# Kernel tuning notes

Hardware: AMD Instinct MI355X
Metric: run time of the kernel (lower is better)

Reference implementation:

```python
import jax, jax.numpy as jnp
import numpy as np

N_TOKENS = 16384
D_MODEL = 1024
N_SEG = 4
H_SEG = 1024  # intermediate_size (4096) // num_segments


def setup_inputs() -> dict:
    key = jax.random.key(0)
    kx, ki, kg, ku, kd = jax.random.split(key, 5)
    x = jax.random.normal(kx, (N_TOKENS, D_MODEL), dtype=jnp.float32)
    token_segment_indices = jax.random.randint(ki, (N_TOKENS,), 0, N_SEG, dtype=jnp.int64)
    s = 1.0 / np.sqrt(D_MODEL)
    # weights stored [seg, in, out] for x @ W
    gate_w = jax.random.normal(kg, (N_SEG, D_MODEL, H_SEG), dtype=jnp.float32) * s
    up_w = jax.random.normal(ku, (N_SEG, D_MODEL, H_SEG), dtype=jnp.float32) * s
    down_w = jax.random.normal(kd, (N_SEG, H_SEG, D_MODEL), dtype=jnp.float32) * (1.0 / np.sqrt(H_SEG))
    return {
        'x': x,
        'gate_w': gate_w,
        'up_w': up_w,
        'down_w': down_w,
        'token_segment_indices': token_segment_indices,
    }


def reference(x, gate_w, up_w, down_w, token_segment_indices):
    # _forward_with_indices: each token is processed only by its assigned
    # segment's SwiGLU FFN; all other contributions are zero.  We compute each
    # segment densely and mask (jit-friendly, same math as gather->ffn->scatter).
    out = jnp.zeros_like(x)
    for s in range(N_SEG):
        hidden = jax.nn.silu(x @ gate_w[s]) * (x @ up_w[s])  # [N, H_SEG]
        y = hidden @ down_w[s]                                # [N, D_MODEL]
        mask = (token_segment_indices == s)[:, None]
        out = out + jnp.where(mask, y, 0.0)
    return out
```

## Files before the change

kernel.cpp:

```cpp
#include <hip/hip_runtime.h>
#include <hip/hip_bf16.h>
#include <math.h>

#define NT   16384
#define DM   1024
#define NSEG 4
#define BK   64
#define HS   1024
#define TBLN 68

typedef __attribute__((ext_vector_type(8))) short bf16x8;
typedef __attribute__((ext_vector_type(4))) float f32x4;

typedef __attribute__((address_space(1))) unsigned int gu32;
typedef __attribute__((address_space(3))) unsigned int lu32;

__device__ __forceinline__ void gll16(const void* g, void* l) {
  __builtin_amdgcn_global_load_lds((gu32*)(unsigned long long)g,
                                   (lu32*)(unsigned int)(unsigned long long)l,
                                   16, 0, 0);
}

__device__ __forceinline__ unsigned short cvt_bf16(float f) {
  unsigned int u = __float_as_uint(f);
  u += 0x7fffu + ((u >> 16) & 1u);
  return (unsigned short)(u >> 16);
}

__global__ __launch_bounds__(256) void k_prepw(
    const int* __restrict__ idx, int* __restrict__ part,
    const float* __restrict__ gw, const float* __restrict__ uw, const float* __restrict__ dw,
    unsigned short* __restrict__ gwt, unsigned short* __restrict__ uwt,
    unsigned short* __restrict__ dwt) {
  __shared__ float tile[64][65];
  const int bid = blockIdx.x, tid = threadIdx.x;
  if (bid < 64) {
    __shared__ int sc[5];
    if (tid < 5) sc[tid] = 0;
    __syncthreads();
    int lane = tid & 63;
    int w32 = idx[bid * 256 + tid];
    unsigned long long m = __ballot((tid & 1) && (w32 != 0));
    if (lane == 0 && m) atomicAdd(&sc[4], 1);
    __syncthreads();
    int is32 = (sc[4] != 0);
    int s = w32;
    if (!is32) s = idx[bid * 512 + 2 * tid];
#pragma unroll
    for (int q = 0; q < 4; ++q) {
      m = __ballot(s == q);
      if (lane == 0 && m) atomicAdd(&sc[q], (int)__popcll(m));
    }
    __syncthreads();
    if (tid < 4) part[bid * 8 + tid] = sc[tid];
    if (tid == 4) part[bid * 8 + 4] = is32;
    return;
  }
  int tb = bid - 64;
  int mtx = tb >> 10, seg = (tb >> 8) & 3, tl = tb & 255;
  const float* src = (mtx == 0 ? gw : mtx == 1 ? uw : dw) + (size_t)seg * DM * HS;
  unsigned short* dst = (mtx == 0 ? gwt : mtx == 1 ? uwt : dwt) + (size_t)seg * DM * HS;
  int n0 = (tl & 15) * 64, k0 = (tl >> 4) * 64;
  int col = tid & 63, rb = tid >> 6;
#pragma unroll
  for (int i = 0; i < 64; i += 4)
    tile[i + rb][col] = src[(size_t)(k0 + i + rb) * 1024 + n0 + col];
  __syncthreads();
  int kp = tid & 31, nb = tid >> 5;
#pragma unroll
  for (int j = 0; j < 64; j += 8) {
    int nn = j + nb;
    unsigned int w = (unsigned)cvt_bf16(tile[2 * kp][nn]) |
                     ((unsigned)cvt_bf16(tile[2 * kp + 1][nn]) << 16);
    *(unsigned int*)(dst + (size_t)(n0 + nn) * 1024 + k0 + 2 * kp) = w;
  }
}

__global__ __launch_bounds__(256) void k_cvtrank(
    const int* __restrict__ idx, const int* __restrict__ part,
    const float4* __restrict__ x,
    int* __restrict__ meta, int2* __restrict__ table,
    int* __restrict__ perm, uint4* __restrict__ xc) {
  __shared__ int cnt[64][4];
  __shared__ int wsum[4][4];
  __shared__ int tot[4], pref[4], gbase[4];
  __shared__ int rnk8[8];
  __shared__ int flag_s;
  const int tid = threadIdx.x, bid = blockIdx.x;
  const int lane = tid & 63, wv = tid >> 6;
  const int c = bid >> 5;
  const int p0 = (bid & 31) * 8;

  if (tid == 0) flag_s = part[c * 8 + 4];
  if (wv == 0) {
#pragma unroll
    for (int s = 0; s < 4; ++s) cnt[lane][s] = part[lane * 8 + s];
  }
  __syncthreads();
  const int is32 = flag_s;
  int tok = c * 256 + tid;
  int s_t = is32 ? idx[tok] : idx[2 * tok];
  int myr = 0;
  unsigned long long lt = (1ull << lane) - 1;
#pragma unroll
  for (int q = 0; q < 4; ++q) {
    unsigned long long m = __ballot(s_t == q);
    if (lane == 0) wsum[wv][q] = (int)__popcll(m);
    if (s_t == q) myr = (int)__popcll(m & lt);
  }
  __syncthreads();
  if (tid < 4) {
    int s = tid, t = 0, p = 0;
    for (int b = 0; b < 64; ++b) { if (b == c) p = t; t += cnt[b][s]; }
    tot[s] = t; pref[s] = p;
  }
  __syncthreads();
  if (tid == 0) {
    gbase[0] = 0;
    for (int s = 1; s < 4; ++s) gbase[s] = gbase[s - 1] + tot[s - 1];
    if (bid == 0) {
      int nt = 0;
      for (int s = 0; s < 4; ++s) {
        meta[s] = tot[s]; meta[5 + s] = gbase[s];
        for (int m0 = 0; m0 < tot[s]; m0 += 256) table[nt++] = make_int2(s, m0);
      }
      for (; nt < TBLN; ++nt) table[nt] = make_int2(-1, 0);
    }
  }
  __syncthreads();
  int wpre = 0;
  for (int w2 = 0; w2 < wv; ++w2) wpre += wsum[w2][s_t];
  int r = gbase[s_t] + pref[s_t] + wpre + myr;
  if (tid >= p0 && tid < p0 + 8) {
    perm[r] = tok;
    rnk8[tid - p0] = r;
  }
  __syncthreads();
  const int j = tid >> 5, l2 = tid & 31;
  const int tok8 = bid * 8 + j;
  const float4* src = x + (size_t)tok8 * 256;
  uint4* dst = xc + (size_t)rnk8[j] * 128;
#pragma unroll
  for (int it = 0; it < 4; ++it) {
    float4 a = src[it * 64 + l2 * 2];
    float4 b = src[it * 64 + l2 * 2 + 1];
    uint4 o;
    o.x = cvt_bf16(a.x) | ((unsigned)cvt_bf16(a.y) << 16);
    o.y = cvt_bf16(a.z) | ((unsigned)cvt_bf16(a.w) << 16);
    o.z = cvt_bf16(b.x) | ((unsigned)cvt_bf16(b.y) << 16);
    o.w = cvt_bf16(b.z) | ((unsigned)cvt_bf16(b.w) << 16);
    dst[it * 32 + l2] = o;
  }
}

#define WAITBAR(N) \
  asm volatile("s_waitcnt vmcnt(" #N ") lgkmcnt(0)\n\ts_barrier" ::: "memory")

#define LDF(BUF, CUR, RB, F)                                               \
  F[0][0] = *(const bf16x8*)(&BUF[CUR][((RB) + fm) * 64] + x0);            \
  F[0][1] = *(const bf16x8*)(&BUF[CUR][((RB) + fm) * 64] + x1);            \
  F[1][0] = *(const bf16x8*)(&BUF[CUR][((RB) + 16 + fm) * 64] + x0);       \
  F[1][1] = *(const bf16x8*)(&BUF[CUR][((RB) + 16 + fm) * 64] + x1);

#define MM8(ACC, MH, NH, AF, BF)                                                                                            \
  __builtin_amdgcn_s_setprio(1);                                                                                            \
  ACC[2*(MH)+0][2*(NH)+0] = __builtin_amdgcn_mfma_f32_16x16x32_bf16(AF[0][0], BF[0][0], ACC[2*(MH)+0][2*(NH)+0], 0, 0, 0);  \
  ACC[2*(MH)+0][2*(NH)+1] = __builtin_amdgcn_mfma_f32_16x16x32_bf16(AF[0][0], BF[1][0], ACC[2*(MH)+0][2*(NH)+1], 0, 0, 0);  \
  ACC[2*(MH)+1][2*(NH)+0] = __builtin_amdgcn_mfma_f32_16x16x32_bf16(AF[1][0], BF[0][0], ACC[2*(MH)+1][2*(NH)+0], 0, 0, 0);  \
  ACC[2*(MH)+1][2*(NH)+1] = __builtin_amdgcn_mfma_f32_16x16x32_bf16(AF[1][0], BF[1][0], ACC[2*(MH)+1][2*(NH)+1], 0, 0, 0);  \
  ACC[2*(MH)+0][2*(NH)+0] = __builtin_amdgcn_mfma_f32_16x16x32_bf16(AF[0][1], BF[0][1], ACC[2*(MH)+0][2*(NH)+0], 0, 0, 0);  \
  ACC[2*(MH)+0][2*(NH)+1] = __builtin_amdgcn_mfma_f32_16x16x32_bf16(AF[0][1], BF[1][1], ACC[2*(MH)+0][2*(NH)+1], 0, 0, 0);  \
  ACC[2*(MH)+1][2*(NH)+0] = __builtin_amdgcn_mfma_f32_16x16x32_bf16(AF[1][1], BF[0][1], ACC[2*(MH)+1][2*(NH)+0], 0, 0, 0);  \
  ACC[2*(MH)+1][2*(NH)+1] = __builtin_amdgcn_mfma_f32_16x16x32_bf16(AF[1][1], BF[1][1], ACC[2*(MH)+1][2*(NH)+1], 0, 0, 0);  \
  __builtin_amdgcn_s_setprio(0);

__global__ __launch_bounds__(512) void k_gateup(
    const unsigned short* __restrict__ xc,
    const unsigned short* __restrict__ gwt,
    const unsigned short* __restrict__ uwt,
    const int* __restrict__ meta,
    const int2* __restrict__ table,
    unsigned short* __restrict__ hidden) {
  __shared__ __align__(16) unsigned short As[2][256 * BK];
  __shared__ __align__(16) unsigned short Bg[2][64 * BK];
  __shared__ __align__(16) unsigned short Bu[2][64 * BK];
  const int bid = blockIdx.x, tid = threadIdx.x;
  const int2 te = table[bid >> 4];
  if (te.x < 0) return;
  const int seg = te.x, m0 = te.y;
  const int count = meta[seg], base = meta[5 + seg];
  const int n0 = (bid & 15) * 64;

  const int lane = tid & 63;
  const int wv = tid >> 6;
  const int l0 = lane >> 3, j = lane & 7;

  const int rl0 = wv * 8, rl1 = 64 + wv * 8;
  const int rb0 = (rl0 & 31) + (rl0 >> 5) * 64;
  const int rb1 = (rl1 & 31) + (rl1 >> 5) * 64;
  const int a0d0 = rb0 * 128, a0d1 = rb1 * 128;
  const int a1d0 = a0d0 + 32 * 128, a1d1 = a0d1 + 32 * 128;
  const int r00 = rb0 + l0, r01 = rb1 + l0;
  const int r10 = r00 + 32, r11 = r01 + 32;
  auto rowof = [&](int r) { int g = m0 + r; return g < count ? g : count - 1; };
  const unsigned short* a0p0 = xc + (size_t)(base + rowof(r00)) * DM + (j ^ (r00 & 7)) * 8;
  const unsigned short* a0p1 = xc + (size_t)(base + rowof(r01)) * DM + (j ^ (r01 & 7)) * 8;
  const unsigned short* a1p0 = xc + (size_t)(base + rowof(r10)) * DM + (j ^ (r10 & 7)) * 8;
  const unsigned short* a1p1 = xc + (size_t)(base + rowof(r11)) * DM + (j ^ (r11 & 7)) * 8;
  const int nb = wv * 8 + l0;
  const unsigned short* gp  = gwt + (size_t)(seg * HS + n0 + nb) * DM + (j ^ (nb & 7)) * 8;
  const unsigned short* upp = uwt + (size_t)(seg * HS + n0 + nb) * DM + (j ^ (nb & 7)) * 8;
  const int bd = wv * 1024;

  const int wm = (wv & 3) * 64;
  const int wn = (wv >> 2) * 32;
  const int fm = lane & 15, fq = lane >> 4;
  const int x0 = (fq ^ (fm & 7)) * 8;
  const int x1 = ((4 + fq) ^ (fm & 7)) * 8;

  f32x4 accg[4][2] = {};
  f32x4 accu[4][2] = {};

#define GU_ITER(CUR, NXT) {                                   \
    bf16x8 af[2][2], af2[2][2], bg2[2][2], bu2[2][2];         \
    gll16(a0p0, (char*)&As[NXT][0] + a0d0);                   \
    gll16(a0p1, (char*)&As[NXT][0] + a0d1);                   \
    WAITBAR(5);                                               \
    LDF(As, CUR, wm, af); LDF(Bg, CUR, wn, bg2);              \
    MM8(accg, 0, 0, af, bg2);                                 \
    gll16(gp, (char*)&Bg[NXT][0] + bd);                       \
    WAITBAR(5);                                               \
    LDF(Bu, CUR, wn, bu2);                                    \
    MM8(accu, 0, 0, af, bu2);                                 \
    gll16(upp, (char*)&Bu[NXT][0] + bd);                      \
    WAITBAR(4);                                               \
    LDF(As, CUR, wm + 32, af2);                               \
    MM8(accg, 1, 0, af2, bg2);                                \
    gll16(a1p0, (char*)&As[NXT][0] + a1d0);                   \
    gll16(a1p1, (char*)&As[NXT][0] + a1d1);                   \
    MM8(accu, 1, 0, af2, bu2);                                \
    a0p0 += BK; a0p1 += BK; a1p0 += BK; a1p1 += BK; gp += BK; upp += BK; \
  }

  gll16(a0p0, (char*)&As[0][0] + a0d0);
  gll16(a0p1, (char*)&As[0][0] + a0d1);
  gll16(gp,   (char*)&Bg[0][0] + bd);
  gll16(upp,  (char*)&Bu[0][0] + bd);
  gll16(a1p0, (char*)&As[0][0] + a1d0);
  gll16(a1p1, (char*)&As[0][0] + a1d1);
  a0p0 += BK; a0p1 += BK; a1p0 += BK; a1p1 += BK; gp += BK; upp += BK;

#pragma unroll 1
  for (int t7 = 0; t7 < 7; ++t7) {
    GU_ITER(0, 1);
    GU_ITER(1, 0);
  }
  GU_ITER(0, 1);
  {
    bf16x8 af[2][2], af2[2][2], bg2[2][2], bu2[2][2];
    WAITBAR(3);
    LDF(As, 1, wm, af); LDF(Bg, 1, wn, bg2);
    MM8(accg, 0, 0, af, bg2);
    WAITBAR(2);
    LDF(Bu, 1, wn, bu2);
    MM8(accu, 0, 0, af, bu2);
    WAITBAR(0);
    LDF(As, 1, wm + 32, af2);
    MM8(accg, 1, 0, af2, bg2);
    MM8(accu, 1, 0, af2, bu2);
  }
#undef GU_ITER

  const int rq = fq * 4;
#pragma unroll
  for (int mi = 0; mi < 4; ++mi) {
#pragma unroll
    for (int r = 0; r < 4; ++r) {
      int row = m0 + wm + mi * 16 + rq + r;
      if (row < count) {
        unsigned short* h = hidden + (size_t)(base + row) * HS + n0 + wn;
#pragma unroll
        for (int ni = 0; ni < 2; ++ni) {
          float gv = accg[mi][ni][r];
          float uv = accu[mi][ni][r];
          float sig = 1.0f / (1.0f + __expf(-gv));
          h[ni * 16 + fm] = cvt_bf16(gv * sig * uv);
        }
      }
    }
  }
}

__global__ __launch_bounds__(512) void k_down(
    const unsigned short* __restrict__ hidden,
    const unsigned short* __restrict__ dwt,
    const int* __restrict__ meta,
    const int2* __restrict__ table,
    const int* __restrict__ perm,
    float* __restrict__ out) {
  __shared__ __align__(16) unsigned short As[2][256 * BK];
  __shared__ __align__(16) unsigned short Bs[2][128 * BK];
  const int bid = blockIdx.x, tid = threadIdx.x;
  const int2 te = table[bid >> 3];
  if (te.x < 0) return;
  const int seg = te.x, m0 = te.y;
  const int count = meta[seg], base = meta[5 + seg];
  const int n0 = (bid & 7) * 128;

  const int lane = tid & 63;
  const int wv = tid >> 6;
  const int l0 = lane >> 3, j = lane & 7;

  const int rl0 = wv * 8, rl1 = 64 + wv * 8;
  const int rb0 = (rl0 & 31) + (rl0 >> 5) * 64;
  const int rb1 = (rl1 & 31) + (rl1 >> 5) * 64;
  const int a0d0 = rb0 * 128, a0d1 = rb1 * 128;
  const int a1d0 = a0d0 + 32 * 128, a1d1 = a0d1 + 32 * 128;
  const int r00 = rb0 + l0, r01 = rb1 + l0;
  const int r10 = r00 + 32, r11 = r01 + 32;
  auto rowof = [&](int r) { int g = m0 + r; return g < count ? g : count - 1; };
  const unsigned short* a0p0 = hidden + (size_t)(base + rowof(r00)) * HS + (j ^ (r00 & 7)) * 8;
  const unsigned short* a0p1 = hidden + (size_t)(base + rowof(r01)) * HS + (j ^ (r01 & 7)) * 8;
  const unsigned short* a1p0 = hidden + (size_t)(base + rowof(r10)) * HS + (j ^ (r10 & 7)) * 8;
  const unsigned short* a1p1 = hidden + (size_t)(base + rowof(r11)) * HS + (j ^ (r11 & 7)) * 8;
  const int nl = wv * 8 + l0;
  const int nb0 = (nl & 31) + (nl >> 5) * 64;
  const int nb1 = nb0 + 32;
  const unsigned short* bp0 = dwt + (size_t)(seg * DM + n0 + nb0) * HS + (j ^ (nb0 & 7)) * 8;
  const unsigned short* bp1 = dwt + (size_t)(seg * DM + n0 + nb1) * HS + (j ^ (nb1 & 7)) * 8;
  const int bw = wv * 8;
  const int bd0 = ((bw & 31) + (bw >> 5) * 64) * 128;
  const int bd1 = bd0 + 32 * 128;

  const int wm = (wv & 3) * 64;
  const int wn = (wv >> 2) * 64;
  const int fm = lane & 15, fq = lane >> 4;
  const int x0 = (fq ^ (fm & 7)) * 8;
  const int x1 = ((4 + fq) ^ (fm & 7)) * 8;

  f32x4 acc[4][4] = {};

#define DN_ITER(CUR, NXT) {                                   \
    bf16x8 af[2][2], af2[2][2], b0[2][2], b1[2][2];           \
    gll16(a0p0, (char*)&As[NXT][0] + a0d0);                   \
    gll16(a0p1, (char*)&As[NXT][0] + a0d1);                   \
    WAITBAR(5);                                               \
    LDF(As, CUR, wm, af); LDF(Bs, CUR, wn, b0);               \
    MM8(acc, 0, 0, af, b0);                                   \
    gll16(bp0, (char*)&Bs[NXT][0] + bd0);                     \
    WAITBAR(5);                                               \
    LDF(Bs, CUR, wn + 32, b1);                                \
    MM8(acc, 0, 1, af, b1);                                   \
    gll16(bp1, (char*)&Bs[NXT][0] + bd1);                     \
    WAITBAR(4);                                               \
    LDF(As, CUR, wm + 32, af2);                               \
    MM8(acc, 1, 0, af2, b0);                                  \
    gll16(a1p0, (char*)&As[NXT][0] + a1d0);                   \
    gll16(a1p1, (char*)&As[NXT][0] + a1d1);                   \
    MM8(acc, 1, 1, af2, b1);                                  \
    a0p0 += BK; a0p1 += BK; a1p0 += BK; a1p1 += BK; bp0 += BK; bp1 += BK; \
  }

  gll16(a0p0, (char*)&As[0][0] + a0d0);
  gll16(a0p1, (char*)&As[0][0] + a0d1);
  gll16(bp0,  (char*)&Bs[0][0] + bd0);
  gll16(bp1,  (char*)&Bs[0][0] + bd1);
  gll16(a1p0, (char*)&As[0][0] + a1d0);
  gll16(a1p1, (char*)&As[0][0] + a1d1);
  a0p0 += BK; a0p1 += BK; a1p0 += BK; a1p1 += BK; bp0 += BK; bp1 += BK;

#pragma unroll 1
  for (int t7 = 0; t7 < 7; ++t7) {
    DN_ITER(0, 1);
    DN_ITER(1, 0);
  }
  DN_ITER(0, 1);
  {
    bf16x8 af[2][2], af2[2][2], b0[2][2], b1[2][2];
    WAITBAR(3);
    LDF(As, 1, wm, af); LDF(Bs, 1, wn, b0);
    MM8(acc, 0, 0, af, b0);
    WAITBAR(2);
    LDF(Bs, 1, wn + 32, b1);
    MM8(acc, 0, 1, af, b1);
    WAITBAR(0);
    LDF(As, 1, wm + 32, af2);
    MM8(acc, 1, 0, af2, b0);
    MM8(acc, 1, 1, af2, b1);
  }
#undef DN_ITER

  const int rq = fq * 4;
#pragma unroll
  for (int mi = 0; mi < 4; ++mi) {
#pragma unroll
    for (int r = 0; r < 4; ++r) {
      int row = m0 + wm + mi * 16 + rq + r;
      if (row < count) {
        int t = perm[base + row];
        float* o = out + (size_t)t * DM + n0 + wn;
#pragma unroll
        for (int ni = 0; ni < 4; ++ni)
          o[ni * 16 + fm] = acc[mi][ni][r];
      }
    }
  }
}


extern "C" void kernel_launch(void* const* d_in, const int* in_sizes, int n_in,
                              void* d_out, int out_size, void* d_ws, size_t ws_size,
                              hipStream_t stream) {
  const float* x  = (const float*)d_in[0];
  const float* gw = (const float*)d_in[1];
  const float* uw = (const float*)d_in[2];
  const float* dw = (const float*)d_in[3];
  const int* tsi  = (const int*)d_in[4];
  float* out = (float*)d_out;

  char* ws = (char*)d_ws;
  int*  meta  = (int*)ws;
  int*  part  = (int*)(ws + 256);
  int2* table = (int2*)(ws + 4096);
  int*  perm  = (int*)(ws + 8192);
  unsigned short* xc  = (unsigned short*)(ws + (1 << 18));
  unsigned short* gwt = xc + (size_t)NT * DM;
  unsigned short* uwt = gwt + (size_t)NSEG * HS * DM;
  unsigned short* dwt = uwt + (size_t)NSEG * HS * DM;
  unsigned short* hid = dwt + (size_t)NSEG * DM * HS;

  k_prepw<<<64 + 3072, 256, 0, stream>>>(tsi, part, gw, uw, dw, gwt, uwt, dwt);
  k_cvtrank<<<2048, 256, 0, stream>>>(tsi, part, (const float4*)x, meta, table, perm, (uint4*)xc);
  k_gateup<<<16 * TBLN, 512, 0, stream>>>(xc, gwt, uwt, meta, table, hid);
  k_down<<<8 * TBLN, 512, 0, stream>>>(hid, dwt, meta, table, perm, out);
}
```

Measured before the change: 307.8 us.

## Triple-buffer LDS in gate/up and down GEMMs for deeper prefetch

Both grouped-GEMM kernels go from double to triple LDS buffering. Two K-tiles are prefetched up front and each iteration issues loads two stages ahead, with the vmcnt waits and the epilogue adjusted to match. The goal is to hide more global-load latency behind MFMA work. In exchange, LDS use per block grows by half, which may lower occupancy; with 512-thread blocks and large tiles this may cost a resident block per CU.

```diff
diff --git a/kernel.cpp b/kernel.cpp
--- a/kernel.cpp
+++ b/kernel.cpp
@@ -153,8 +153,9 @@
   }
 }
 
-#define WAITBAR(N) \
+#define WAITBAR_(N) \
   asm volatile("s_waitcnt vmcnt(" #N ") lgkmcnt(0)\n\ts_barrier" ::: "memory")
+#define WAITBAR(N) WAITBAR_(N)
 
 #define LDF(BUF, CUR, RB, F)                                               \
   F[0][0] = *(const bf16x8*)(&BUF[CUR][((RB) + fm) * 64] + x0);            \
@@ -181,9 +182,9 @@
     const int* __restrict__ meta,
     const int2* __restrict__ table,
     unsigned short* __restrict__ hidden) {
-  __shared__ __align__(16) unsigned short As[2][256 * BK];
-  __shared__ __align__(16) unsigned short Bg[2][64 * BK];
-  __shared__ __align__(16) unsigned short Bu[2][64 * BK];
+  __shared__ __align__(16) unsigned short As[3][256 * BK];
+  __shared__ __align__(16) unsigned short Bg[3][64 * BK];
+  __shared__ __align__(16) unsigned short Bu[3][64 * BK];
   const int bid = blockIdx.x, tid = threadIdx.x;
   const int2 te = table[bid >> 4];
   if (te.x < 0) return;
@@ -221,55 +222,65 @@
   f32x4 accg[4][2] = {};
   f32x4 accu[4][2] = {};
 
-#define GU_ITER(CUR, NXT) {                                   \
+#define GU_STAGE(B) {                                         \
+    gll16(a0p0, (char*)&As[B][0] + a0d0);                     \
+    gll16(a0p1, (char*)&As[B][0] + a0d1);                     \
+    gll16(gp,   (char*)&Bg[B][0] + bd);                       \
+    gll16(upp,  (char*)&Bu[B][0] + bd);                       \
+    gll16(a1p0, (char*)&As[B][0] + a1d0);                     \
+    gll16(a1p1, (char*)&As[B][0] + a1d1);                     \
+    a0p0 += BK; a0p1 += BK; a1p0 += BK; a1p1 += BK; gp += BK; upp += BK; \
+  }
+
+#define GU_ITER(C, P) {                                       \
     bf16x8 af[2][2], af2[2][2], bg2[2][2], bu2[2][2];         \
-    gll16(a0p0, (char*)&As[NXT][0] + a0d0);                   \
-    gll16(a0p1, (char*)&As[NXT][0] + a0d1);                   \
-    WAITBAR(5);                                               \
-    LDF(As, CUR, wm, af); LDF(Bg, CUR, wn, bg2);              \
+    gll16(a0p0, (char*)&As[P][0] + a0d0);                     \
+    gll16(a0p1, (char*)&As[P][0] + a0d1);                     \
+    WAITBAR(11);                                              \
+    LDF(As, C, wm, af); LDF(Bg, C, wn, bg2);                  \
     MM8(accg, 0, 0, af, bg2);                                 \
-    gll16(gp, (char*)&Bg[NXT][0] + bd);                       \
-    WAITBAR(5);                                               \
-    LDF(Bu, CUR, wn, bu2);                                    \
+    gll16(gp, (char*)&Bg[P][0] + bd);                         \
+    WAITBAR(11);                                              \
+    LDF(Bu, C, wn, bu2);                                      \
     MM8(accu, 0, 0, af, bu2);                                 \
-    gll16(upp, (char*)&Bu[NXT][0] + bd);                      \
-    WAITBAR(4);                                               \
-    LDF(As, CUR, wm + 32, af2);                               \
+    gll16(upp, (char*)&Bu[P][0] + bd);                        \
+    WAITBAR(10);                                              \
+    LDF(As, C, wm + 32, af2);                                 \
     MM8(accg, 1, 0, af2, bg2);                                \
-    gll16(a1p0, (char*)&As[NXT][0] + a1d0);                   \
-    gll16(a1p1, (char*)&As[NXT][0] + a1d1);                   \
+    gll16(a1p0, (char*)&As[P][0] + a1d0);                     \
+    gll16(a1p1, (char*)&As[P][0] + a1d1);                     \
     MM8(accu, 1, 0, af2, bu2);                                \
     a0p0 += BK; a0p1 += BK; a1p0 += BK; a1p1 += BK; gp += BK; upp += BK; \
   }
 
-  gll16(a0p0, (char*)&As[0][0] + a0d0);
-  gll16(a0p1, (char*)&As[0][0] + a0d1);
-  gll16(gp,   (char*)&Bg[0][0] + bd);
-  gll16(upp,  (char*)&Bu[0][0] + bd);
-  gll16(a1p0, (char*)&As[0][0] + a1d0);
-  gll16(a1p1, (char*)&As[0][0] + a1d1);
-  a0p0 += BK; a0p1 += BK; a1p0 += BK; a1p1 += BK; gp += BK; upp += BK;
+#define GU_EPI(C, W1, W2, W3) {                               \
+    bf16x8 af[2][2], af2[2][2], bg2[2][2], bu2[2][2];         \
+    WAITBAR(W1);                                              \
+    LDF(As, C, wm, af); LDF(Bg, C, wn, bg2);                  \
+    MM8(accg, 0, 0, af, bg2);                                 \
+    WAITBAR(W2);                                              \
+    LDF(Bu, C, wn, bu2);                                      \
+    MM8(accu, 0, 0, af, bu2);                                 \
+    WAITBAR(W3);                                              \
+    LDF(As, C, wm + 32, af2);                                 \
+    MM8(accg, 1, 0, af2, bg2);                                \
+    MM8(accu, 1, 0, af2, bu2);                                \
+  }
+
+  GU_STAGE(0);
+  GU_STAGE(1);
 
 #pragma unroll 1
-  for (int t7 = 0; t7 < 7; ++t7) {
-    GU_ITER(0, 1);
-    GU_ITER(1, 0);
-  }
-  GU_ITER(0, 1);
-  {
-    bf16x8 af[2][2], af2[2][2], bg2[2][2], bu2[2][2];
-    WAITBAR(3);
-    LDF(As, 1, wm, af); LDF(Bg, 1, wn, bg2);
-    MM8(accg, 0, 0, af, bg2);
-    WAITBAR(2);
-    LDF(Bu, 1, wn, bu2);
-    MM8(accu, 0, 0, af, bu2);
-    WAITBAR(0);
-    LDF(As, 1, wm + 32, af2);
-    MM8(accg, 1, 0, af2, bg2);
-    MM8(accu, 1, 0, af2, bu2);
-  }
+  for (int g3 = 0; g3 < 4; ++g3) {
+    GU_ITER(0, 2); GU_ITER(1, 0); GU_ITER(2, 1);
+  }
+  GU_ITER(0, 2);
+  GU_ITER(1, 0);
+  GU_EPI(2, 9, 8, 6);
+  GU_EPI(0, 3, 2, 0);
 #undef GU_ITER
+#undef GU_EPI
+#undef GU_STAGE
 
   const int rq = fq * 4;
 #pragma unroll
@@ -298,8 +309,8 @@
     const int2* __restrict__ table,
     const int* __restrict__ perm,
     float* __restrict__ out) {
-  __shared__ __align__(16) unsigned short As[2][256 * BK];
-  __shared__ __align__(16) unsigned short Bs[2][128 * BK];
+  __shared__ __align__(16) unsigned short As[3][256 * BK];
+  __shared__ __align__(16) unsigned short Bs[3][128 * BK];
   const int bid = blockIdx.x, tid = threadIdx.x;
   const int2 te = table[bid >> 3];
   if (te.x < 0) return;
@@ -340,55 +351,65 @@
 
   f32x4 acc[4][4] = {};
 
-#define DN_ITER(CUR, NXT) {                                   \
+#define DN_STAGE(B) {                                         \
+    gll16(a0p0, (char*)&As[B][0] + a0d0);                     \
+    gll16(a0p1, (char*)&As[B][0] + a0d1);                     \
+    gll16(bp0,  (char*)&Bs[B][0] + bd0);                      \
+    gll16(bp1,  (char*)&Bs[B][0] + bd1);                      \
+    gll16(a1p0, (char*)&As[B][0] + a1d0);                     \
+    gll16(a1p1, (char*)&As[B][0] + a1d1);                     \
+    a0p0 += BK; a0p1 += BK; a1p0 += BK; a1p1 += BK; bp0 += BK; bp1 += BK; \
+  }
+
+#define DN_ITER(C, P) {                                       \
     bf16x8 af[2][2], af2[2][2], b0[2][2], b1[2][2];           \
-    gll16(a0p0, (char*)&As[NXT][0] + a0d0);                   \
-    gll16(a0p1, (char*)&As[NXT][0] + a0d1);                   \
-    WAITBAR(5);                                               \
-    LDF(As, CUR, wm, af); LDF(Bs, CUR, wn, b0);               \
+    gll16(a0p0, (char*)&As[P][0] + a0d0);                     \
+    gll16(a0p1, (char*)&As[P][0] + a0d1);                     \
+    WAITBAR(11);                                              \
+    LDF(As, C, wm, af); LDF(Bs, C, wn, b0);                   \
     MM8(acc, 0, 0, af, b0);                                   \
-    gll16(bp0, (char*)&Bs[NXT][0] + bd0);                     \
-    WAITBAR(5);                                               \
-    LDF(Bs, CUR, wn + 32, b1);                                \
+    gll16(bp0, (char*)&Bs[P][0] + bd0);                       \
+    WAITBAR(11);                                              \
+    LDF(Bs, C, wn + 32, b1);                                  \
     MM8(acc, 0, 1, af, b1);                                   \
-    gll16(bp1, (char*)&Bs[NXT][0] + bd1);                     \
-    WAITBAR(4);                                               \
-    LDF(As, CUR, wm + 32, af2);                               \
+    gll16(bp1, (char*)&Bs[P][0] + bd1);                       \
+    WAITBAR(10);                                              \
+    LDF(As, C, wm + 32, af2);                                 \
     MM8(acc, 1, 0, af2, b0);                                  \
-    gll16(a1p0, (char*)&As[NXT][0] + a1d0);                   \
-    gll16(a1p1, (char*)&As[NXT][0] + a1d1);                   \
+    gll16(a1p0, (char*)&As[P][0] + a1d0);                     \
+    gll16(a1p1, (char*)&As[P][0] + a1d1);                     \
     MM8(acc, 1, 1, af2, b1);                                  \
     a0p0 += BK; a0p1 += BK; a1p0 += BK; a1p1 += BK; bp0 += BK; bp1 += BK; \
   }
 
-  gll16(a0p0, (char*)&As[0][0] + a0d0);
-  gll16(a0p1, (char*)&As[0][0] + a0d1);
-  gll16(bp0,  (char*)&Bs[0][0] + bd0);
-  gll16(bp1,  (char*)&Bs[0][0] + bd1);
-  gll16(a1p0, (char*)&As[0][0] + a1d0);
-  gll16(a1p1, (char*)&As[0][0] + a1d1);
-  a0p0 += BK; a0p1 += BK; a1p0 += BK; a1p1 += BK; bp0 += BK; bp1 += BK;
+#define DN_EPI(C, W1, W2, W3) {                               \
+    bf16x8 af[2][2], af2[2][2], b0[2][2], b1[2][2];           \
+    WAITBAR(W1);                                              \
+    LDF(As, C, wm, af); LDF(Bs, C, wn, b0);                   \
+    MM8(acc, 0, 0, af, b0);                                   \
+    WAITBAR(W2);                                              \
+    LDF(Bs, C, wn + 32, b1);                                  \
+    MM8(acc, 0, 1, af, b1);                                   \
+    WAITBAR(W3);                                              \
+    LDF(As, C, wm + 32, af2);                                 \
+    MM8(acc, 1, 0, af2, b0);                                  \
+    MM8(acc, 1, 1, af2, b1);                                  \
+  }
+
+  DN_STAGE(0);
+  DN_STAGE(1);
 
 #pragma unroll 1
-  for (int t7 = 0; t7 < 7; ++t7) {
-    DN_ITER(0, 1);
-    DN_ITER(1, 0);
-  }
-  DN_ITER(0, 1);
-  {
-    bf16x8 af[2][2], af2[2][2], b0[2][2], b1[2][2];
-    WAITBAR(3);
-    LDF(As, 1, wm, af); LDF(Bs, 1, wn, b0);
-    MM8(acc, 0, 0, af, b0);
-    WAITBAR(2);
-    LDF(Bs, 1, wn + 32, b1);
-    MM8(acc, 0, 1, af, b1);
-    WAITBAR(0);
-    LDF(As, 1, wm + 32, af2);
-    MM8(acc, 1, 0, af2, b0);
-    MM8(acc, 1, 1, af2, b1);
-  }
+  for (int g3 = 0; g3 < 4; ++g3) {
+    DN_ITER(0, 2); DN_ITER(1, 0); DN_ITER(2, 1);
+  }
+  DN_ITER(0, 2);
+  DN_ITER(1, 0);
+  DN_EPI(2, 9, 8, 6);
+  DN_EPI(0, 3, 2, 0);
 #undef DN_ITER
+#undef DN_EPI
+#undef DN_STAGE
 
   const int rq = fq * 4;
 #pragma unroll
```

Result: no change. 312.2 us (+1.4%).
